# Kernel optimization log

Hardware: AMD Instinct MI355X
Metric: run time of the kernel (lower is better)

Reference implementation:

```python
import jax, jax.numpy as jnp
import numpy as np

N_NODES = 100000
N_EDGES = 600000
N_RBF = 6
EMBED_DIM = 128
VOCAB = 100  # nn.Embedding(100, embed_dim, padding_idx=0)


def setup_inputs() -> dict:
    key = jax.random.key(0)
    k1, k2, k3, k4, k5, k6, k7 = jax.random.split(key, 7)
    e_rbf = jax.random.normal(k1, (N_EDGES, N_RBF), dtype=jnp.float32)
    z = jax.random.randint(k2, (N_NODES,), 0, VOCAB, dtype=jnp.int64)
    nbr_list = jax.random.randint(k3, (N_EDGES, 2), 0, N_NODES, dtype=jnp.int64)
    # params
    W_edge = jax.random.normal(k4, (N_RBF, EMBED_DIM), dtype=jnp.float32) / np.sqrt(N_RBF)
    emb_table = jax.random.normal(k5, (VOCAB, EMBED_DIM), dtype=jnp.float32)
    emb_table = emb_table.at[0].set(0.0)  # padding_idx=0
    W_dense = jax.random.normal(k6, (3 * EMBED_DIM, EMBED_DIM), dtype=jnp.float32) / np.sqrt(3 * EMBED_DIM)
    b_dense = jax.random.normal(k7, (EMBED_DIM,), dtype=jnp.float32) * 0.01
    return {"e_rbf": e_rbf, "z": z, "nbr_list": nbr_list,
            "W_edge": W_edge, "emb_table": emb_table,
            "W_dense": W_dense, "b_dense": b_dense}


def reference(e_rbf, z, nbr_list, W_edge, emb_table, W_dense, b_dense):
    # edge_dense: [E, n_rbf] @ [n_rbf, D] -> [E, D], no bias, no activation
    e = e_rbf @ W_edge
    # node embedding lookup: [N, D]
    h = emb_table[z]
    # gather + concat: [E, 3D]
    m_ji = jnp.concatenate((h[nbr_list[:, 0]], h[nbr_list[:, 1]], e), axis=-1)
    # dense 3D -> D with bias, then swish (silu) activation
    m_ji = jax.nn.silu(m_ji @ W_dense + b_dense)
    return m_ji
```

## Files before the change

kernel.cpp:

```cpp
#include <hip/hip_runtime.h>
#include <hip/hip_fp16.h>

#define EMBED 128
#define NRBF 6
#define VOCAB 100
#define EBLOCK 1024
#define GROUPS 32
#define CPG 37
#define HALF (GROUPS * CPG)
#define BCHUNK (2 * HALF)
#define TABLE_F (VOCAB * EMBED * 2 + NRBF * EMBED)
#define SMEM_BYTES (TABLE_F * 4 + HALF * 16)

__global__ __launch_bounds__(EMBED) void precompute_kernel(
    const float* __restrict__ W_edge,
    const float* __restrict__ emb,
    const float* __restrict__ Wd,
    const float* __restrict__ b,
    float* __restrict__ T1,
    float* __restrict__ T2,
    float* __restrict__ Wc)
{
    const int d = threadIdx.x;
    const int v = blockIdx.x;
    if (v < 2 * VOCAB) {
        const int row = (v < VOCAB) ? v : v - VOCAB;
        const int woff = (v < VOCAB) ? 0 : EMBED;
        __shared__ float hrow[EMBED];
        hrow[d] = emb[row * EMBED + d];
        __syncthreads();
        float acc = (v < VOCAB) ? b[d] : 0.0f;
        #pragma unroll 8
        for (int j = 0; j < EMBED; ++j)
            acc += hrow[j] * Wd[(woff + j) * EMBED + d];
        if (v < VOCAB) T1[row * EMBED + d] = acc;
        else           T2[row * EMBED + d] = acc;
    } else {
        const int k = v - 2 * VOCAB;
        float acc = 0.0f;
        #pragma unroll 8
        for (int j = 0; j < EMBED; ++j)
            acc += W_edge[k * EMBED + j] * Wd[(2 * EMBED + j) * EMBED + d];
        Wc[k * EMBED + d] = acc;
    }
}

__global__ __launch_bounds__(EBLOCK) void edge_kernel(
    const float* __restrict__ e_rbf,
    const int*   __restrict__ z,
    const int*   __restrict__ nbr,
    const float* __restrict__ tables,
    float* __restrict__ out,
    int E)
{
    extern __shared__ float smem[];
    float* T1s = smem;
    float* T2s = smem + VOCAB * EMBED;
    float* Wcs = smem + 2 * VOCAB * EMBED;
    uint4* meta = (uint4*)(smem + TABLE_F);

    const int tid  = threadIdx.x;
    const int base = blockIdx.x * BCHUNK;
    const int lane = tid & 31;
    const int d    = lane * 4;
    const int g    = tid >> 5;

    {
        const float4* src = reinterpret_cast<const float4*>(tables);
        float4* dst = reinterpret_cast<float4*>(smem);
        #pragma unroll 2
        for (int i = tid; i < TABLE_F / 4; i += EBLOCK)
            dst[i] = src[i];
    }

    {
        for (int s = 0; s < 2; ++s) {
            const int idx = tid + s * EBLOCK;
            if (idx >= HALF) break;
            const int e = base + idx;
            uint4 m = make_uint4(0u, 0u, 0u, 0u);
            if (e < E) {
                const int2 nn = *reinterpret_cast<const int2*>(nbr + 2 * e);
                const float* rp = e_rbf + (long)e * NRBF;
                const float2 a = *reinterpret_cast<const float2*>(rp + 0);
                const float2 bb = *reinterpret_cast<const float2*>(rp + 2);
                const float2 c = *reinterpret_cast<const float2*>(rp + 4);
                __half2 ha = __float22half2_rn(a);
                __half2 hb = __float22half2_rn(bb);
                __half2 hc = __float22half2_rn(c);
                m.x = *reinterpret_cast<unsigned*>(&ha);
                m.y = *reinterpret_cast<unsigned*>(&hb);
                m.z = *reinterpret_cast<unsigned*>(&hc);
                m.w = (unsigned)z[nn.x] | ((unsigned)z[nn.y] << 16);
            }
            meta[idx] = m;
        }
    }

    int2  nnA = make_int2(0, 0);
    float2 rA0 = make_float2(0.f, 0.f), rA1 = rA0, rA2 = rA0;
    int2  nnB = make_int2(0, 0);
    float2 rB0 = make_float2(0.f, 0.f), rB1 = rB0, rB2 = rB0;
    const int eA = base + HALF + tid;
    const bool vA = (eA < E);
    const int eB = base + HALF + EBLOCK + tid;
    const bool vB = (tid < HALF - EBLOCK) && (eB < E);
    if (vA) {
        nnA = *reinterpret_cast<const int2*>(nbr + 2 * eA);
        const float* rp = e_rbf + (long)eA * NRBF;
        rA0 = *reinterpret_cast<const float2*>(rp + 0);
        rA1 = *reinterpret_cast<const float2*>(rp + 2);
        rA2 = *reinterpret_cast<const float2*>(rp + 4);
    }
    if (vB) {
        nnB = *reinterpret_cast<const int2*>(nbr + 2 * eB);
        const float* rp = e_rbf + (long)eB * NRBF;
        rB0 = *reinterpret_cast<const float2*>(rp + 0);
        rB1 = *reinterpret_cast<const float2*>(rp + 2);
        rB2 = *reinterpret_cast<const float2*>(rp + 4);
    }
    __syncthreads();

    const float4 wc0 = *reinterpret_cast<const float4*>(Wcs + 0 * EMBED + d);
    const float4 wc1 = *reinterpret_cast<const float4*>(Wcs + 1 * EMBED + d);
    const float4 wc2 = *reinterpret_cast<const float4*>(Wcs + 2 * EMBED + d);
    const float4 wc3 = *reinterpret_cast<const float4*>(Wcs + 3 * EMBED + d);
    const float4 wc4 = *reinterpret_cast<const float4*>(Wcs + 4 * EMBED + d);
    const float4 wc5 = *reinterpret_cast<const float4*>(Wcs + 5 * EMBED + d);

    auto consume_half = [&](int ebase) {
        const int lb = (g >> 1) * (2 * CPG) + (g & 1);
        #pragma unroll 4
        for (int i = 0; i < CPG; ++i) {
            const int le = lb + 2 * i;
            const int e = ebase + le;
            if (e >= E) break;

            const uint4 m = meta[le];
            const float2 f01 = __half22float2(*reinterpret_cast<const __half2*>(&m.x));
            const float2 f23 = __half22float2(*reinterpret_cast<const __half2*>(&m.y));
            const float2 f45 = __half22float2(*reinterpret_cast<const __half2*>(&m.z));
            const int za = (int)(m.w & 0xffffu) << 7;
            const int zb = (int)(m.w >> 16) << 7;

            float4 acc = *reinterpret_cast<const float4*>(T1s + za + d);
            const float4 t2 = *reinterpret_cast<const float4*>(T2s + zb + d);
            acc.x += t2.x; acc.y += t2.y; acc.z += t2.z; acc.w += t2.w;

            acc.x += f01.x * wc0.x; acc.y += f01.x * wc0.y; acc.z += f01.x * wc0.z; acc.w += f01.x * wc0.w;
            acc.x += f01.y * wc1.x; acc.y += f01.y * wc1.y; acc.z += f01.y * wc1.z; acc.w += f01.y * wc1.w;
            acc.x += f23.x * wc2.x; acc.y += f23.x * wc2.y; acc.z += f23.x * wc2.z; acc.w += f23.x * wc2.w;
            acc.x += f23.y * wc3.x; acc.y += f23.y * wc3.y; acc.z += f23.y * wc3.z; acc.w += f23.y * wc3.w;
            acc.x += f45.x * wc4.x; acc.y += f45.x * wc4.y; acc.z += f45.x * wc4.z; acc.w += f45.x * wc4.w;
            acc.x += f45.y * wc5.x; acc.y += f45.y * wc5.y; acc.z += f45.y * wc5.z; acc.w += f45.y * wc5.w;

            float4 rr;
            rr.x = acc.x * __builtin_amdgcn_rcpf(1.0f + __expf(-acc.x));
            rr.y = acc.y * __builtin_amdgcn_rcpf(1.0f + __expf(-acc.y));
            rr.z = acc.z * __builtin_amdgcn_rcpf(1.0f + __expf(-acc.z));
            rr.w = acc.w * __builtin_amdgcn_rcpf(1.0f + __expf(-acc.w));

            *reinterpret_cast<float4*>(out + (long)e * EMBED + d) = rr;
        }
    };

    consume_half(base);
    __syncthreads();

    {
        if (tid < HALF) {
            uint4 m = make_uint4(0u, 0u, 0u, 0u);
            if (vA) {
                __half2 ha = __float22half2_rn(rA0);
                __half2 hb = __float22half2_rn(rA1);
                __half2 hc = __float22half2_rn(rA2);
                m.x = *reinterpret_cast<unsigned*>(&ha);
                m.y = *reinterpret_cast<unsigned*>(&hb);
                m.z = *reinterpret_cast<unsigned*>(&hc);
                m.w = (unsigned)z[nnA.x] | ((unsigned)z[nnA.y] << 16);
            }
            meta[tid] = m;
        }
        if (tid < HALF - EBLOCK) {
            uint4 m = make_uint4(0u, 0u, 0u, 0u);
            if (vB) {
                __half2 ha = __float22half2_rn(rB0);
                __half2 hb = __float22half2_rn(rB1);
                __half2 hc = __float22half2_rn(rB2);
                m.x = *reinterpret_cast<unsigned*>(&ha);
                m.y = *reinterpret_cast<unsigned*>(&hb);
                m.z = *reinterpret_cast<unsigned*>(&hc);
                m.w = (unsigned)z[nnB.x] | ((unsigned)z[nnB.y] << 16);
            }
            meta[EBLOCK + tid] = m;
        }
    }
    __syncthreads();

    consume_half(base + HALF);
}

extern "C" void kernel_launch(void* const* d_in, const int* in_sizes, int n_in,
                              void* d_out, int out_size, void* d_ws, size_t ws_size,
                              hipStream_t stream)
{
    const float* e_rbf  = (const float*)d_in[0];
    const int*   z      = (const int*)  d_in[1];
    const int*   nbr    = (const int*)  d_in[2];
    const float* W_edge = (const float*)d_in[3];
    const float* emb    = (const float*)d_in[4];
    const float* Wd     = (const float*)d_in[5];
    const float* b      = (const float*)d_in[6];
    float* out = (float*)d_out;

    const int E = in_sizes[2] / 2;

    float* T1 = (float*)d_ws;
    float* T2 = T1 + VOCAB * EMBED;
    float* Wc = T2 + VOCAB * EMBED;

    precompute_kernel<<<2 * VOCAB + NRBF, EMBED, 0, stream>>>(W_edge, emb, Wd, b, T1, T2, Wc);

    const int grid = (E + BCHUNK - 1) / BCHUNK;
    edge_kernel<<<grid, EBLOCK, SMEM_BYTES, stream>>>(e_rbf, z, nbr, T1, out, E);
}
```

Measured before the change: 78.96 us.

## Split edge packing into separate kernel and stream metadata with double buffering

A new pack kernel gathers z indices and converts e_rbf to half into a workspace metadata array. The edge kernel then runs as a persistent grid of 256 blocks, each walking its edge range in 512-edge chunks. The next chunk's metadata is prefetched into a double-buffered shared-memory slot while the current one is consumed. Table lookups are software-pipelined one iteration ahead. This amortizes the per-block table copy across more edges and removes the gather latency from the main loop, at the cost of an extra kernel launch and a global round trip for the metadata, with a fallback path if the workspace is too small.

Measured after the change: 84.67 us. +7.2%, slower.

```diff
diff --git a/kernel.cpp b/kernel.cpp
--- a/kernel.cpp
+++ b/kernel.cpp
@@ -5,12 +5,16 @@
 #define NRBF 6
 #define VOCAB 100
 #define EBLOCK 1024
+#define EGRID 256
+#define CHUNK 512
+#define PC (CHUNK / 32)
+#define TABLE_F (VOCAB * EMBED * 2 + NRBF * EMBED)
+#define SMEM_MAIN (TABLE_F * 4 + 2 * CHUNK * 16)
 #define GROUPS 32
 #define CPG 37
-#define HALF (GROUPS * CPG)
-#define BCHUNK (2 * HALF)
-#define TABLE_F (VOCAB * EMBED * 2 + NRBF * EMBED)
-#define SMEM_BYTES (TABLE_F * 4 + HALF * 16)
+#define HALF_E (GROUPS * CPG)
+#define BCHUNK (2 * HALF_E)
+#define SMEM_FB (TABLE_F * 4 + HALF_E * 16)
 
 __global__ __launch_bounds__(EMBED) void precompute_kernel(
     const float* __restrict__ W_edge,
@@ -45,25 +49,51 @@
     }
 }
 
-__global__ __launch_bounds__(EBLOCK) void edge_kernel(
+__global__ __launch_bounds__(256) void pack_kernel(
     const float* __restrict__ e_rbf,
     const int*   __restrict__ z,
     const int*   __restrict__ nbr,
+    uint4* __restrict__ meta, int E, int Epad)
+{
+    const int e = blockIdx.x * 256 + threadIdx.x;
+    if (e >= Epad) return;
+    uint4 m = make_uint4(0u, 0u, 0u, 0u);
+    if (e < E) {
+        const int2 nn = *reinterpret_cast<const int2*>(nbr + 2 * e);
+        const float* rp = e_rbf + (long)e * NRBF;
+        const float2 a = *reinterpret_cast<const float2*>(rp + 0);
+        const float2 bb = *reinterpret_cast<const float2*>(rp + 2);
+        const float2 c = *reinterpret_cast<const float2*>(rp + 4);
+        __half2 ha = __float22half2_rn(a);
+        __half2 hb = __float22half2_rn(bb);
+        __half2 hc = __float22half2_rn(c);
+        m.x = *reinterpret_cast<unsigned*>(&ha);
+        m.y = *reinterpret_cast<unsigned*>(&hb);
+        m.z = *reinterpret_cast<unsigned*>(&hc);
+        m.w = (unsigned)z[nn.x] | ((unsigned)z[nn.y] << 16);
+    }
+    meta[e] = m;
+}
+
+__global__ __launch_bounds__(EBLOCK) void edge_kernel(
+    const uint4* __restrict__ meta_g,
     const float* __restrict__ tables,
     float* __restrict__ out,
-    int E)
+    int E, int BCH, int NCH)
 {
     extern __shared__ float smem[];
     float* T1s = smem;
     float* T2s = smem + VOCAB * EMBED;
     float* Wcs = smem + 2 * VOCAB * EMBED;
-    uint4* meta = (uint4*)(smem + TABLE_F);
+    uint4* buf0 = (uint4*)(smem + TABLE_F);
+    uint4* buf1 = buf0 + CHUNK;
 
     const int tid  = threadIdx.x;
-    const int base = blockIdx.x * BCHUNK;
+    const int base = blockIdx.x * BCH;
     const int lane = tid & 31;
     const int d    = lane * 4;
     const int g    = tid >> 5;
+    const uint4* mg = meta_g + base;
 
     {
         const float4* src = reinterpret_cast<const float4*>(tables);
@@ -71,40 +101,138 @@
         #pragma unroll 2
         for (int i = tid; i < TABLE_F / 4; i += EBLOCK)
             dst[i] = src[i];
-    }
+        if (tid < CHUNK)
+            buf0[tid] = (tid < BCH) ? mg[tid] : make_uint4(0u, 0u, 0u, 0u);
+    }
+    __syncthreads();
+
+    const float4 wc0 = *reinterpret_cast<const float4*>(Wcs + 0 * EMBED + d);
+    const float4 wc1 = *reinterpret_cast<const float4*>(Wcs + 1 * EMBED + d);
+    const float4 wc2 = *reinterpret_cast<const float4*>(Wcs + 2 * EMBED + d);
+    const float4 wc3 = *reinterpret_cast<const float4*>(Wcs + 3 * EMBED + d);
+    const float4 wc4 = *reinterpret_cast<const float4*>(Wcs + 4 * EMBED + d);
+    const float4 wc5 = *reinterpret_cast<const float4*>(Wcs + 5 * EMBED + d);
+
+    const int minE = min(BCH, E - base);
+    const int lb = ((g >> 1) << 5) + (g & 1);
+
+    int cur = 0;
+    for (int c = 0; c < NCH; ++c) {
+        uint4 nx = make_uint4(0u, 0u, 0u, 0u);
+        const bool have = (c + 1 < NCH) && (tid < CHUNK);
+        if (have) {
+            const int idx = (c + 1) * CHUNK + tid;
+            if (idx < BCH) nx = mg[idx];
+        }
+
+        const uint4* bufc = (cur == 0) ? buf0 : buf1;
+        const int lim = minE - c * CHUNK;
+        const int ebase = base + c * CHUNK;
+
+        uint4 m0 = bufc[lb];
+        uint4 m1 = bufc[lb + 2];
+        float4 t1 = *reinterpret_cast<const float4*>(T1s + (((int)(m0.w & 0xffffu)) << 7) + d);
+        float4 t2 = *reinterpret_cast<const float4*>(T2s + (((int)(m0.w >> 16)) << 7) + d);
+
+        #pragma unroll
+        for (int i = 0; i < PC; ++i) {
+            float4 t1n = t1, t2n = t2;
+            uint4 m2 = m1;
+            if (i + 1 < PC) {
+                t1n = *reinterpret_cast<const float4*>(T1s + (((int)(m1.w & 0xffffu)) << 7) + d);
+                t2n = *reinterpret_cast<const float4*>(T2s + (((int)(m1.w >> 16)) << 7) + d);
+            }
+            if (i + 2 < PC) m2 = bufc[lb + 2 * (i + 2)];
+
+            const float2 f01 = __half22float2(*reinterpret_cast<const __half2*>(&m0.x));
+            const float2 f23 = __half22float2(*reinterpret_cast<const __half2*>(&m0.y));
+            const float2 f45 = __half22float2(*reinterpret_cast<const __half2*>(&m0.z));
+
+            float4 acc = t1;
+            acc.x += t2.x; acc.y += t2.y; acc.z += t2.z; acc.w += t2.w;
+            acc.x += f01.x * wc0.x; acc.y += f01.x * wc0.y; acc.z += f01.x * wc0.z; acc.w += f01.x * wc0.w;
+            acc.x += f01.y * wc1.x; acc.y += f01.y * wc1.y; acc.z += f01.y * wc1.z; acc.w += f01.y * wc1.w;
+            acc.x += f23.x * wc2.x; acc.y += f23.x * wc2.y; acc.z += f23.x * wc2.z; acc.w += f23.x * wc2.w;
+            acc.x += f23.y * wc3.x; acc.y += f23.y * wc3.y; acc.z += f23.y * wc3.z; acc.w += f23.y * wc3.w;
+            acc.x += f45.x * wc4.x; acc.y += f45.x * wc4.y; acc.z += f45.x * wc4.z; acc.w += f45.x * wc4.w;
+            acc.x += f45.y * wc5.x; acc.y += f45.y * wc5.y; acc.z += f45.y * wc5.z; acc.w += f45.y * wc5.w;
+
+            float4 rr;
+            rr.x = acc.x * __builtin_amdgcn_rcpf(1.0f + __expf(-acc.x));
+            rr.y = acc.y * __builtin_amdgcn_rcpf(1.0f + __expf(-acc.y));
+            rr.z = acc.z * __builtin_amdgcn_rcpf(1.0f + __expf(-acc.z));
+            rr.w = acc.w * __builtin_amdgcn_rcpf(1.0f + __expf(-acc.w));
+
+            const int le = lb + 2 * i;
+            if (le < lim)
+                *reinterpret_cast<float4*>(out + (long)(ebase + le) * EMBED + d) = rr;
+
+            m0 = m1; m1 = m2; t1 = t1n; t2 = t2n;
+        }
+
+        uint4* bufn = (cur == 0) ? buf1 : buf0;
+        if (have) bufn[tid] = nx;
+        __syncthreads();
+        cur ^= 1;
+    }
+}
+
+__global__ __launch_bounds__(EBLOCK) void edge_kernel_fb(
+    const float* __restrict__ e_rbf,
+    const int*   __restrict__ z,
+    const int*   __restrict__ nbr,
+    const float* __restrict__ tables,
+    float* __restrict__ out, int E)
+{
+    extern __shared__ float smem[];
+    float* T1s = smem;
+    float* T2s = smem + VOCAB * EMBED;
+    float* Wcs = smem + 2 * VOCAB * EMBED;
+    uint4* meta = (uint4*)(smem + TABLE_F);
+
+    const int tid  = threadIdx.x;
+    const int base = blockIdx.x * BCHUNK;
+    const int lane = tid & 31;
+    const int d    = lane * 4;
+    const int g    = tid >> 5;
 
     {
-        for (int s = 0; s < 2; ++s) {
-            const int idx = tid + s * EBLOCK;
-            if (idx >= HALF) break;
-            const int e = base + idx;
-            uint4 m = make_uint4(0u, 0u, 0u, 0u);
-            if (e < E) {
-                const int2 nn = *reinterpret_cast<const int2*>(nbr + 2 * e);
-                const float* rp = e_rbf + (long)e * NRBF;
-                const float2 a = *reinterpret_cast<const float2*>(rp + 0);
-                const float2 bb = *reinterpret_cast<const float2*>(rp + 2);
-                const float2 c = *reinterpret_cast<const float2*>(rp + 4);
-                __half2 ha = __float22half2_rn(a);
-                __half2 hb = __float22half2_rn(bb);
-                __half2 hc = __float22half2_rn(c);
-                m.x = *reinterpret_cast<unsigned*>(&ha);
-                m.y = *reinterpret_cast<unsigned*>(&hb);
-                m.z = *reinterpret_cast<unsigned*>(&hc);
-                m.w = (unsigned)z[nn.x] | ((unsigned)z[nn.y] << 16);
-            }
-            meta[idx] = m;
-        }
-    }
-
-    int2  nnA = make_int2(0, 0);
+        const float4* src = reinterpret_cast<const float4*>(tables);
+        float4* dst = reinterpret_cast<float4*>(smem);
+        #pragma unroll 2
+        for (int i = tid; i < TABLE_F / 4; i += EBLOCK)
+            dst[i] = src[i];
+    }
+    for (int s = 0; s < 2; ++s) {
+        const int idx = tid + s * EBLOCK;
+        if (idx >= HALF_E) break;
+        const int e = base + idx;
+        uint4 m = make_uint4(0u, 0u, 0u, 0u);
+        if (e < E) {
+            const int2 nn = *reinterpret_cast<const int2*>(nbr + 2 * e);
+            const float* rp = e_rbf + (long)e * NRBF;
+            const float2 a = *reinterpret_cast<const float2*>(rp + 0);
+            const float2 bb = *reinterpret_cast<const float2*>(rp + 2);
+            const float2 c = *reinterpret_cast<const float2*>(rp + 4);
+            __half2 ha = __float22half2_rn(a);
+            __half2 hb = __float22half2_rn(bb);
+            __half2 hc = __float22half2_rn(c);
+            m.x = *reinterpret_cast<unsigned*>(&ha);
+            m.y = *reinterpret_cast<unsigned*>(&hb);
+            m.z = *reinterpret_cast<unsigned*>(&hc);
+            m.w = (unsigned)z[nn.x] | ((unsigned)z[nn.y] << 16);
+        }
+        meta[idx] = m;
+    }
+
+    int2 nnA = make_int2(0, 0);
     float2 rA0 = make_float2(0.f, 0.f), rA1 = rA0, rA2 = rA0;
-    int2  nnB = make_int2(0, 0);
+    int2 nnB = make_int2(0, 0);
     float2 rB0 = make_float2(0.f, 0.f), rB1 = rB0, rB2 = rB0;
-    const int eA = base + HALF + tid;
+    const int eA = base + HALF_E + tid;
     const bool vA = (eA < E);
-    const int eB = base + HALF + EBLOCK + tid;
-    const bool vB = (tid < HALF - EBLOCK) && (eB < E);
+    const int eB = base + HALF_E + EBLOCK + tid;
+    const bool vB = (tid < HALF_E - EBLOCK) && (eB < E);
     if (vA) {
         nnA = *reinterpret_cast<const int2*>(nbr + 2 * eA);
         const float* rp = e_rbf + (long)eA * NRBF;
@@ -135,7 +263,6 @@
             const int le = lb + 2 * i;
             const int e = ebase + le;
             if (e >= E) break;
-
             const uint4 m = meta[le];
             const float2 f01 = __half22float2(*reinterpret_cast<const __half2*>(&m.x));
             const float2 f23 = __half22float2(*reinterpret_cast<const __half2*>(&m.y));
@@ -146,7 +273,6 @@
             float4 acc = *reinterpret_cast<const float4*>(T1s + za + d);
             const float4 t2 = *reinterpret_cast<const float4*>(T2s + zb + d);
             acc.x += t2.x; acc.y += t2.y; acc.z += t2.z; acc.w += t2.w;
-
             acc.x += f01.x * wc0.x; acc.y += f01.x * wc0.y; acc.z += f01.x * wc0.z; acc.w += f01.x * wc0.w;
             acc.x += f01.y * wc1.x; acc.y += f01.y * wc1.y; acc.z += f01.y * wc1.z; acc.w += f01.y * wc1.w;
             acc.x += f23.x * wc2.x; acc.y += f23.x * wc2.y; acc.z += f23.x * wc2.z; acc.w += f23.x * wc2.w;
@@ -159,45 +285,40 @@
             rr.y = acc.y * __builtin_amdgcn_rcpf(1.0f + __expf(-acc.y));
             rr.z = acc.z * __builtin_amdgcn_rcpf(1.0f + __expf(-acc.z));
             rr.w = acc.w * __builtin_amdgcn_rcpf(1.0f + __expf(-acc.w));
-
             *reinterpret_cast<float4*>(out + (long)e * EMBED + d) = rr;
         }
     };
 
     consume_half(base);
     __syncthreads();
-
-    {
-        if (tid < HALF) {
-            uint4 m = make_uint4(0u, 0u, 0u, 0u);
-            if (vA) {
-                __half2 ha = __float22half2_rn(rA0);
-                __half2 hb = __float22half2_rn(rA1);
-                __half2 hc = __float22half2_rn(rA2);
-                m.x = *reinterpret_cast<unsigned*>(&ha);
-                m.y = *reinterpret_cast<unsigned*>(&hb);
-                m.z = *reinterpret_cast<unsigned*>(&hc);
-                m.w = (unsigned)z[nnA.x] | ((unsigned)z[nnA.y] << 16);
-            }
-            meta[tid] = m;
-        }
-        if (tid < HALF - EBLOCK) {
-            uint4 m = make_uint4(0u, 0u, 0u, 0u);
-            if (vB) {
-                __half2 ha = __float22half2_rn(rB0);
-                __half2 hb = __float22half2_rn(rB1);
-                __half2 hc = __float22half2_rn(rB2);
-                m.x = *reinterpret_cast<unsigned*>(&ha);
-                m.y = *reinterpret_cast<unsigned*>(&hb);
-                m.z = *reinterpret_cast<unsigned*>(&hc);
-                m.w = (unsigned)z[nnB.x] | ((unsigned)z[nnB.y] << 16);
-            }
-            meta[EBLOCK + tid] = m;
-        }
+    if (tid < HALF_E) {
+        uint4 m = make_uint4(0u, 0u, 0u, 0u);
+        if (vA) {
+            __half2 ha = __float22half2_rn(rA0);
+            __half2 hb = __float22half2_rn(rA1);
+            __half2 hc = __float22half2_rn(rA2);
+            m.x = *reinterpret_cast<unsigned*>(&ha);
+            m.y = *reinterpret_cast<unsigned*>(&hb);
+            m.z = *reinterpret_cast<unsigned*>(&hc);
+            m.w = (unsigned)z[nnA.x] | ((unsigned)z[nnA.y] << 16);
+        }
+        meta[tid] = m;
+    }
+    if (tid < HALF_E - EBLOCK) {
+        uint4 m = make_uint4(0u, 0u, 0u, 0u);
+        if (vB) {
+            __half2 ha = __float22half2_rn(rB0);
+            __half2 hb = __float22half2_rn(rB1);
+            __half2 hc = __float22half2_rn(rB2);
+            m.x = *reinterpret_cast<unsigned*>(&ha);
+            m.y = *reinterpret_cast<unsigned*>(&hb);
+            m.z = *reinterpret_cast<unsigned*>(&hc);
+            m.w = (unsigned)z[nnB.x] | ((unsigned)z[nnB.y] << 16);
+        }
+        meta[EBLOCK + tid] = m;
     }
     __syncthreads();
-
-    consume_half(base + HALF);
+    consume_half(base + HALF_E);
 }
 
 extern "C" void kernel_launch(void* const* d_in, const int* in_sizes, int n_in,
@@ -218,9 +339,20 @@
     float* T1 = (float*)d_ws;
     float* T2 = T1 + VOCAB * EMBED;
     float* Wc = T2 + VOCAB * EMBED;
+    uint4* meta = (uint4*)((char*)d_ws + TABLE_F * 4);
 
     precompute_kernel<<<2 * VOCAB + NRBF, EMBED, 0, stream>>>(W_edge, emb, Wd, b, T1, T2, Wc);
 
-    const int grid = (E + BCHUNK - 1) / BCHUNK;
-    edge_kernel<<<grid, EBLOCK, SMEM_BYTES, stream>>>(e_rbf, z, nbr, T1, out, E);
-}
+    const int BCH  = (E + EGRID - 1) / EGRID;
+    const int NCH  = (BCH + CHUNK - 1) / CHUNK;
+    const int Epad = EGRID * BCH;
+    const size_t need = (size_t)TABLE_F * 4 + (size_t)Epad * 16;
+
+    if (ws_size >= need) {
+        pack_kernel<<<(Epad + 255) / 256, 256, 0, stream>>>(e_rbf, z, nbr, meta, E, Epad);
+        edge_kernel<<<EGRID, EBLOCK, SMEM_MAIN, stream>>>(meta, T1, out, E, BCH, NCH);
+    } else {
+        const int grid = (E + BCHUNK - 1) / BCHUNK;
+        edge_kernel_fb<<<grid, EBLOCK, SMEM_FB, stream>>>(e_rbf, z, nbr, T1, out, E);
+    }
+}
```

## Store node-projection tables in fp16 in LDS and shrink per-block edge chunk

Applied to the files above, without the earlier changes.

The precomputed T1/T2 node tables are stored as half precision, roughly halving their LDS footprint and the bytes each block copies in. The per-block chunk is cut from 2x37 to 2x19 edges per group, the register prefetch of the second half is replaced by staging it after the first half is consumed, and the inner loop is fully unrolled with the bounds check moved to the store. Smaller LDS use should let more blocks share a CU, but it adds fp16 rounding to the table values and makes each block copy the tables for fewer edges.

Result: faster. 75.38 us (median of 2 runs) (-4.5%).

```diff
diff --git a/kernel.cpp b/kernel.cpp
--- a/kernel.cpp
+++ b/kernel.cpp
@@ -6,19 +6,20 @@
 #define VOCAB 100
 #define EBLOCK 1024
 #define GROUPS 32
-#define CPG 37
-#define HALF (GROUPS * CPG)
-#define BCHUNK (2 * HALF)
-#define TABLE_F (VOCAB * EMBED * 2 + NRBF * EMBED)
-#define SMEM_BYTES (TABLE_F * 4 + HALF * 16)
+#define CPG 19
+#define HALF_E (GROUPS * CPG / 2 * 2)
+#define BCHUNK (2 * HALF_E)
+#define T_HALFS (VOCAB * EMBED)
+#define TABLE_BYTES (2 * T_HALFS * 2 + NRBF * EMBED * 4)
+#define SMEM_BYTES (TABLE_BYTES + HALF_E * 16)
 
 __global__ __launch_bounds__(EMBED) void precompute_kernel(
     const float* __restrict__ W_edge,
     const float* __restrict__ emb,
     const float* __restrict__ Wd,
     const float* __restrict__ b,
-    float* __restrict__ T1,
-    float* __restrict__ T2,
+    __half* __restrict__ T1h,
+    __half* __restrict__ T2h,
     float* __restrict__ Wc)
 {
     const int d = threadIdx.x;
@@ -33,8 +34,8 @@
         #pragma unroll 8
         for (int j = 0; j < EMBED; ++j)
             acc += hrow[j] * Wd[(woff + j) * EMBED + d];
-        if (v < VOCAB) T1[row * EMBED + d] = acc;
-        else           T2[row * EMBED + d] = acc;
+        if (v < VOCAB) T1h[row * EMBED + d] = __float2half_rn(acc);
+        else           T2h[row * EMBED + d] = __float2half_rn(acc);
     } else {
         const int k = v - 2 * VOCAB;
         float acc = 0.0f;
@@ -45,7 +46,7 @@
     }
 }
 
-__global__ __launch_bounds__(EBLOCK) void edge_kernel(
+__global__ __launch_bounds__(EBLOCK, 8) void edge_kernel(
     const float* __restrict__ e_rbf,
     const int*   __restrict__ z,
     const int*   __restrict__ nbr,
@@ -53,11 +54,11 @@
     float* __restrict__ out,
     int E)
 {
-    extern __shared__ float smem[];
-    float* T1s = smem;
-    float* T2s = smem + VOCAB * EMBED;
-    float* Wcs = smem + 2 * VOCAB * EMBED;
-    uint4* meta = (uint4*)(smem + TABLE_F);
+    extern __shared__ char smemraw[];
+    __half* T1s = (__half*)smemraw;
+    __half* T2s = T1s + T_HALFS;
+    float*  Wcs = (float*)(smemraw + 2 * T_HALFS * 2);
+    uint4*  meta = (uint4*)(smemraw + TABLE_BYTES);
 
     const int tid  = threadIdx.x;
     const int base = blockIdx.x * BCHUNK;
@@ -67,24 +68,22 @@
 
     {
         const float4* src = reinterpret_cast<const float4*>(tables);
-        float4* dst = reinterpret_cast<float4*>(smem);
+        float4* dst = reinterpret_cast<float4*>(smemraw);
         #pragma unroll 2
-        for (int i = tid; i < TABLE_F / 4; i += EBLOCK)
+        for (int i = tid; i < TABLE_BYTES / 16; i += EBLOCK)
             dst[i] = src[i];
     }
 
-    {
-        for (int s = 0; s < 2; ++s) {
-            const int idx = tid + s * EBLOCK;
-            if (idx >= HALF) break;
-            const int e = base + idx;
+    auto stage_half = [&](int ebase) {
+        if (tid < HALF_E) {
+            const int e = ebase + tid;
             uint4 m = make_uint4(0u, 0u, 0u, 0u);
             if (e < E) {
                 const int2 nn = *reinterpret_cast<const int2*>(nbr + 2 * e);
                 const float* rp = e_rbf + (long)e * NRBF;
-                const float2 a = *reinterpret_cast<const float2*>(rp + 0);
+                const float2 a  = *reinterpret_cast<const float2*>(rp + 0);
                 const float2 bb = *reinterpret_cast<const float2*>(rp + 2);
-                const float2 c = *reinterpret_cast<const float2*>(rp + 4);
+                const float2 c  = *reinterpret_cast<const float2*>(rp + 4);
                 __half2 ha = __float22half2_rn(a);
                 __half2 hb = __float22half2_rn(bb);
                 __half2 hc = __float22half2_rn(c);
@@ -93,32 +92,11 @@
                 m.z = *reinterpret_cast<unsigned*>(&hc);
                 m.w = (unsigned)z[nn.x] | ((unsigned)z[nn.y] << 16);
             }
-            meta[idx] = m;
+            meta[tid] = m;
         }
-    }
+    };
 
-    int2  nnA = make_int2(0, 0);
-    float2 rA0 = make_float2(0.f, 0.f), rA1 = rA0, rA2 = rA0;
-    int2  nnB = make_int2(0, 0);
-    float2 rB0 = make_float2(0.f, 0.f), rB1 = rB0, rB2 = rB0;
-    const int eA = base + HALF + tid;
-    const bool vA = (eA < E);
-    const int eB = base + HALF + EBLOCK + tid;
-    const bool vB = (tid < HALF - EBLOCK) && (eB < E);
-    if (vA) {
-        nnA = *reinterpret_cast<const int2*>(nbr + 2 * eA);
-        const float* rp = e_rbf + (long)eA * NRBF;
-        rA0 = *reinterpret_cast<const float2*>(rp + 0);
-        rA1 = *reinterpret_cast<const float2*>(rp + 2);
-        rA2 = *reinterpret_cast<const float2*>(rp + 4);
-    }
-    if (vB) {
-        nnB = *reinterpret_cast<const int2*>(nbr + 2 * eB);
-        const float* rp = e_rbf + (long)eB * NRBF;
-        rB0 = *reinterpret_cast<const float2*>(rp + 0);
-        rB1 = *reinterpret_cast<const float2*>(rp + 2);
-        rB2 = *reinterpret_cast<const float2*>(rp + 4);
-    }
+    stage_half(base);
     __syncthreads();
 
     const float4 wc0 = *reinterpret_cast<const float4*>(Wcs + 0 * EMBED + d);
@@ -130,22 +108,28 @@
 
     auto consume_half = [&](int ebase) {
         const int lb = (g >> 1) * (2 * CPG) + (g & 1);
-        #pragma unroll 4
+        #pragma unroll
         for (int i = 0; i < CPG; ++i) {
             const int le = lb + 2 * i;
             const int e = ebase + le;
-            if (e >= E) break;
 
             const uint4 m = meta[le];
+            const int za = (int)(m.w & 0xffffu) << 7;
+            const int zb = (int)(m.w >> 16) << 7;
+
+            const uint2 t1p = *reinterpret_cast<const uint2*>(T1s + za + d);
+            const uint2 t2p = *reinterpret_cast<const uint2*>(T2s + zb + d);
+            const __half2 s0 = __hadd2(*reinterpret_cast<const __half2*>(&t1p.x),
+                                       *reinterpret_cast<const __half2*>(&t2p.x));
+            const __half2 s1 = __hadd2(*reinterpret_cast<const __half2*>(&t1p.y),
+                                       *reinterpret_cast<const __half2*>(&t2p.y));
+            const float2 a01 = __half22float2(s0);
+            const float2 a23 = __half22float2(s1);
+            float4 acc = make_float4(a01.x, a01.y, a23.x, a23.y);
+
             const float2 f01 = __half22float2(*reinterpret_cast<const __half2*>(&m.x));
             const float2 f23 = __half22float2(*reinterpret_cast<const __half2*>(&m.y));
             const float2 f45 = __half22float2(*reinterpret_cast<const __half2*>(&m.z));
-            const int za = (int)(m.w & 0xffffu) << 7;
-            const int zb = (int)(m.w >> 16) << 7;
-
-            float4 acc = *reinterpret_cast<const float4*>(T1s + za + d);
-            const float4 t2 = *reinterpret_cast<const float4*>(T2s + zb + d);
-            acc.x += t2.x; acc.y += t2.y; acc.z += t2.z; acc.w += t2.w;
 
             acc.x += f01.x * wc0.x; acc.y += f01.x * wc0.y; acc.z += f01.x * wc0.z; acc.w += f01.x * wc0.w;
             acc.x += f01.y * wc1.x; acc.y += f01.y * wc1.y; acc.z += f01.y * wc1.z; acc.w += f01.y * wc1.w;
@@ -160,44 +144,17 @@
             rr.z = acc.z * __builtin_amdgcn_rcpf(1.0f + __expf(-acc.z));
             rr.w = acc.w * __builtin_amdgcn_rcpf(1.0f + __expf(-acc.w));
 
-            *reinterpret_cast<float4*>(out + (long)e * EMBED + d) = rr;
+            if (e < E)
+                *reinterpret_cast<float4*>(out + (long)e * EMBED + d) = rr;
         }
     };
 
     consume_half(base);
     __syncthreads();
 
-    {
-        if (tid < HALF) {
-            uint4 m = make_uint4(0u, 0u, 0u, 0u);
-            if (vA) {
-                __half2 ha = __float22half2_rn(rA0);
-                __half2 hb = __float22half2_rn(rA1);
-                __half2 hc = __float22half2_rn(rA2);
-                m.x = *reinterpret_cast<unsigned*>(&ha);
-                m.y = *reinterpret_cast<unsigned*>(&hb);
-                m.z = *reinterpret_cast<unsigned*>(&hc);
-                m.w = (unsigned)z[nnA.x] | ((unsigned)z[nnA.y] << 16);
-            }
-            meta[tid] = m;
-        }
-        if (tid < HALF - EBLOCK) {
-            uint4 m = make_uint4(0u, 0u, 0u, 0u);
-            if (vB) {
-                __half2 ha = __float22half2_rn(rB0);
-                __half2 hb = __float22half2_rn(rB1);
-                __half2 hc = __float22half2_rn(rB2);
-                m.x = *reinterpret_cast<unsigned*>(&ha);
-                m.y = *reinterpret_cast<unsigned*>(&hb);
-                m.z = *reinterpret_cast<unsigned*>(&hc);
-                m.w = (unsigned)z[nnB.x] | ((unsigned)z[nnB.y] << 16);
-            }
-            meta[EBLOCK + tid] = m;
-        }
-    }
+    stage_half(base + HALF_E);
     __syncthreads();
-
-    consume_half(base + HALF);
+    consume_half(base + HALF_E);
 }
 
 extern "C" void kernel_launch(void* const* d_in, const int* in_sizes, int n_in,
@@ -215,12 +172,12 @@
 
     const int E = in_sizes[2] / 2;
 
-    float* T1 = (float*)d_ws;
-    float* T2 = T1 + VOCAB * EMBED;
-    float* Wc = T2 + VOCAB * EMBED;
+    __half* T1h = (__half*)d_ws;
+    __half* T2h = T1h + T_HALFS;
+    float*  Wc  = (float*)((char*)d_ws + 2 * T_HALFS * 2);
 
-    precompute_kernel<<<2 * VOCAB + NRBF, EMBED, 0, stream>>>(W_edge, emb, Wd, b, T1, T2, Wc);
+    precompute_kernel<<<2 * VOCAB + NRBF, EMBED, 0, stream>>>(W_edge, emb, Wd, b, T1h, T2h, Wc);
 
     const int grid = (E + BCHUNK - 1) / BCHUNK;
-    edge_kernel<<<grid, EBLOCK, SMEM_BYTES, stream>>>(e_rbf, z, nbr, T1, out, E);
+    edge_kernel<<<grid, EBLOCK, SMEM_BYTES, stream>>>(e_rbf, z, nbr, (const float*)d_ws, out, E);
 }
```
